# Optimization experiments

Measured on AMD Instinct MI355X. Metric: run time of the kernel, lower is better.

Reference implementation:

```python
import jax, jax.numpy as jnp
import numpy as np

B, F, H, S, K, L, C = 128, 8192, 8192, 4, 32, 3, 100  # batch, encoded feats, hidden, segments, synapses/seg, hidden layers, classes


def setup_inputs() -> dict:
    key = jax.random.key(0)
    k1, k2, k3, k4, k5, k6 = jax.random.split(key, 6)
    # binary encoded input activations (thermometer-coded tabular features)
    x = jax.random.randint(k1, (B, F), 0, 2).astype(jnp.float32)
    # sign weights in {-1,+1} for each synapse of each segment of each neuron
    signs0 = jnp.where(jax.random.bernoulli(k2, 0.5, (S, H, K)), 1.0, -1.0).astype(jnp.float32)
    signsH = jnp.where(jax.random.bernoulli(k3, 0.5, (L - 1, S, H, K)), 1.0, -1.0).astype(jnp.float32)
    # synapse source indices (irregular connectivity)
    idx0 = jax.random.randint(k4, (S, H, K), 0, F, dtype=jnp.int32)
    idxH = jax.random.randint(k5, (L - 1, S, H, K), 0, H, dtype=jnp.int32)
    # per-layer output connection matrices [L, H, C]
    wout = jax.random.normal(k6, (L, H, C), dtype=jnp.float32) * 0.02
    return {"x": x, "signs0": signs0, "signsH": signsH, "wout": wout,
            "idx0": idx0, "idxH": idxH, "threshold": 8}


def _segment_layer(a, idx, signs, threshold):
    # a: [B, P] prev activations; idx/signs: [S, H, K]
    g = a[:, idx]                                  # [B, S, H, K] irregular gather
    z = jnp.einsum('bshk,shk->bsh', g, signs)      # per-segment summed input
    fired = jnp.any(z >= threshold, axis=1)        # OR over segments -> [B, H]
    return fired.astype(a.dtype)


def reference(x, signs0, signsH, wout, idx0, idxH, threshold):
    thr = jnp.float32(threshold)
    a = _segment_layer(x, idx0, signs0, thr)       # hidden layer 0
    acts = [a]
    for l in range(idxH.shape[0]):                 # remaining hidden layers (fixed small L)
        a = _segment_layer(a, idxH[l], signsH[l], thr)
        acts.append(a)
    # sum class votes from every hidden layer's output connection matrix
    out = jnp.einsum('lbh,lhc->bc', jnp.stack(acts, 0), wout)  # [B, C]
    return out
```

## Files before the change

kernel.cpp:

```cpp
#include <hip/hip_runtime.h>
#include <stdint.h>

#define B 128
#define F 8192
#define H 8192
#define S 4
#define K 32
#define L 3
#define C 100

#define NBLK 256
#define NTHR 512


__device__ __forceinline__ int load_threshold(const int* p) {
    int v = *p;
    if (v >= (1 << 23)) v = (int)__int_as_float(v);
    return v;
}

__device__ __forceinline__ void cs5(uint32_t* a, uint32_t v) {
#pragma unroll
    for (int i = 0; i < 5; ++i) { const uint32_t t = a[i]; a[i] = t ^ v; v = t & v; }
}

__device__ __forceinline__ void pair_sum5(const uint32_t* x, uint32_t* y) {
    uint32_t c = 0;
#pragma unroll
    for (int i = 0; i < 5; ++i) {
        const uint32_t p = (uint32_t)__shfl_xor((int)x[i], 32);
        const uint32_t s = x[i] ^ p;
        y[i] = s ^ c;
        c = (x[i] & p) | (s & c);
    }
    y[5] = c;
}

__device__ __forceinline__ uint32_t fired_cmp(const uint32_t* A, const uint32_t* P, int thr) {
    uint32_t Y[7];
    uint32_t c = 0;
#pragma unroll
    for (int i = 0; i < 7; ++i) {
        const uint32_t ai = (i < 6) ? A[i] : 0u;
        const uint32_t bm = ((thr >> i) & 1) ? 0xFFFFFFFFu : 0u;
        const uint32_t t  = ai ^ bm;
        Y[i] = t ^ c;
        c = (ai & bm) | (t & c);
    }
    uint32_t bw = 0;
#pragma unroll
    for (int i = 0; i < 7; ++i) {
        const uint32_t xx = (i >= 1) ? P[i - 1] : 0u;
        const uint32_t d  = xx ^ Y[i];
        bw = ((~xx) & Y[i]) | ((~d) & bw);
    }
    return ~bw;
}

#define GLDS16(gp, lp)                                                \
    __builtin_amdgcn_global_load_lds(                                 \
        (const __attribute__((address_space(1))) uint32_t*)(gp),      \
        (__attribute__((address_space(3))) uint32_t*)(lp), 16, 0, 0)

#define AG_LOAD(p)                                                          \
    __hip_atomic_load((p), __ATOMIC_RELAXED, __HIP_MEMORY_SCOPE_AGENT)
#define AG_STORE(p, v)                                                      \
    __hip_atomic_store((p), (v), __ATOMIC_RELAXED, __HIP_MEMORY_SCOPE_AGENT)

__device__ __forceinline__ void wp_barrier(uint32_t* wbar, uint32_t ep,
                                           int tid, int gidx) {
    asm volatile("s_waitcnt vmcnt(0)" ::: "memory");
    __syncthreads();
    if (tid == 0) {
        const uint32_t t = __hip_atomic_fetch_add(&wbar[gidx * 16], 1u,
                               __ATOMIC_RELAXED, __HIP_MEMORY_SCOPE_AGENT) + 1u;
        if (t == ep * 16u) {
            const uint32_t r = __hip_atomic_fetch_add(&wbar[128], 1u,
                               __ATOMIC_RELAXED, __HIP_MEMORY_SCOPE_AGENT) + 1u;
            if (r == ep * 8u) AG_STORE(&wbar[160], ep);
        }
        int guard = 0;
        while (AG_LOAD(&wbar[160]) < ep) {
            __builtin_amdgcn_s_sleep(2);
            if (++guard > (1 << 17)) break;
        }
    }
    __syncthreads();
    asm volatile("" ::: "memory");
}

__device__ __forceinline__ void layer_phase(
        const uint32_t* __restrict__ prevPlane,
        const int* __restrict__ idx,
        const float* __restrict__ signs,
        uint32_t* __restrict__ outPlane,
        const int thr, const int hg, const int tid,
        uint2* tab, uint32_t* fbuf) {
    const int lane = tid & 63;
    const int ww   = tid >> 6;
    const int s    = ww & 3;
    const int rh   = ww >> 2;
    const int kh   = lane >> 5;
    const int h5   = lane & 31;
    const int hloc = rh * 32 + h5;
    const int h    = hg * 64 + hloc;

    const size_t gb = ((size_t)s * H + h) * K + kh * 16;
    const int4   i0 = *(const int4*)(idx + gb);
    const int4   i1 = *(const int4*)(idx + gb + 4);
    const int4   i2 = *(const int4*)(idx + gb + 8);
    const int4   i3 = *(const int4*)(idx + gb + 12);
    const float4 s0 = *(const float4*)(signs + gb);
    const float4 s1 = *(const float4*)(signs + gb + 4);
    const float4 s2 = *(const float4*)(signs + gb + 8);
    const float4 s3 = *(const float4*)(signs + gb + 12);

    {
        uint32_t* lbase = (uint32_t*)tab;
#pragma unroll
        for (int i = 0; i < 8; ++i) {
            const int o = (i * 512 + tid) * 4;
            GLDS16(prevPlane + o, lbase + o);
        }
    }
    __syncthreads();

    const uint32_t iv[16] = {
        (uint32_t)i0.x, (uint32_t)i0.y, (uint32_t)i0.z, (uint32_t)i0.w,
        (uint32_t)i1.x, (uint32_t)i1.y, (uint32_t)i1.z, (uint32_t)i1.w,
        (uint32_t)i2.x, (uint32_t)i2.y, (uint32_t)i2.z, (uint32_t)i2.w,
        (uint32_t)i3.x, (uint32_t)i3.y, (uint32_t)i3.z, (uint32_t)i3.w };
    const uint32_t pm[16] = {
        ~(uint32_t)(__float_as_int(s0.x) >> 31), ~(uint32_t)(__float_as_int(s0.y) >> 31),
        ~(uint32_t)(__float_as_int(s0.z) >> 31), ~(uint32_t)(__float_as_int(s0.w) >> 31),
        ~(uint32_t)(__float_as_int(s1.x) >> 31), ~(uint32_t)(__float_as_int(s1.y) >> 31),
        ~(uint32_t)(__float_as_int(s1.z) >> 31), ~(uint32_t)(__float_as_int(s1.w) >> 31),
        ~(uint32_t)(__float_as_int(s2.x) >> 31), ~(uint32_t)(__float_as_int(s2.y) >> 31),
        ~(uint32_t)(__float_as_int(s2.z) >> 31), ~(uint32_t)(__float_as_int(s2.w) >> 31),
        ~(uint32_t)(__float_as_int(s3.x) >> 31), ~(uint32_t)(__float_as_int(s3.y) >> 31),
        ~(uint32_t)(__float_as_int(s3.z) >> 31), ~(uint32_t)(__float_as_int(s3.w) >> 31) };

    uint32_t A0[5] = {0,0,0,0,0}, P0[5] = {0,0,0,0,0};
    uint32_t A1[5] = {0,0,0,0,0}, P1[5] = {0,0,0,0,0};
#pragma unroll
    for (int c8 = 0; c8 < 2; ++c8) {
        uint2 g[8];
#pragma unroll
        for (int j = 0; j < 8; ++j) g[j] = tab[iv[c8 * 8 + j]];
#pragma unroll
        for (int j = 0; j < 8; ++j) {
            const uint32_t pmv = pm[c8 * 8 + j];
            cs5(A0, g[j].x);
            cs5(P0, g[j].x & pmv);
            cs5(A1, g[j].y);
            cs5(P1, g[j].y & pmv);
        }
    }

    uint32_t A0f[6], P0f[6], A1f[6], P1f[6];
    pair_sum5(A0, A0f);
    pair_sum5(P0, P0f);
    pair_sum5(A1, A1f);
    pair_sum5(P1, P1f);

    const uint32_t f0 = fired_cmp(A0f, P0f, thr);
    const uint32_t f1 = fired_cmp(A1f, P1f, thr);

    if (kh == 0) {
        fbuf[((s * 2 + rh) * 32 + h5) * 2 + 0] = f0;
        fbuf[((s * 2 + rh) * 32 + h5) * 2 + 1] = f1;
    }
    __syncthreads();

    if (tid < 128) {
        const int rr   = tid >> 6;
        const int hh   = (tid >> 1) & 31;
        const int comp = tid & 1;
        uint32_t v = 0;
#pragma unroll
        for (int s2 = 0; s2 < 4; ++s2)
            v |= fbuf[((s2 * 2 + rr) * 32 + hh) * 2 + comp];
        AG_STORE(&outPlane[(size_t)(hg * 64 + rr * 32 + hh) * 2 + comp], v);
    }
}

__global__ __launch_bounds__(128) void init_pack_kernel(
        const float* __restrict__ x, uint2* __restrict__ xPP,
        float* __restrict__ out, uint32_t* __restrict__ bar) {
    const int zi = blockIdx.x * 128 + threadIdx.x;
    if (zi < B * C) out[zi] = 0.0f;
    if (blockIdx.x < 4) bar[blockIdx.x * 128 + threadIdx.x] = 0u;

    const int b  = threadIdx.x;
    const int wv = threadIdx.x >> 6;
    const int f0 = blockIdx.x * 32;
    const float4* xr = (const float4*)(x + (size_t)b * F + f0);
    for (int j = 0; j < 8; ++j) {
        const float4 v = xr[j];
        const uint64_t m0 = __ballot(v.x > 0.5f);
        const uint64_t m1 = __ballot(v.y > 0.5f);
        const uint64_t m2 = __ballot(v.z > 0.5f);
        const uint64_t m3 = __ballot(v.w > 0.5f);
        if ((threadIdx.x & 63) == 0) {
            const int f = f0 + 4 * j;
            uint4* dst = (uint4*)(xPP + (size_t)wv * F + f);
            dst[0] = make_uint4((uint32_t)m0, (uint32_t)(m0 >> 32),
                                (uint32_t)m1, (uint32_t)(m1 >> 32));
            dst[1] = make_uint4((uint32_t)m2, (uint32_t)(m2 >> 32),
                                (uint32_t)m3, (uint32_t)(m3 >> 32));
        }
    }
}

__global__ __launch_bounds__(512, 4) void fused_kernel(
        const uint32_t* __restrict__ xPP,
        const int* __restrict__ idx0, const float* __restrict__ signs0,
        const int* __restrict__ idxH, const float* __restrict__ signsH,
        const float* __restrict__ wout, const int* __restrict__ thrp,
        uint32_t* __restrict__ actPP, float* __restrict__ out,
        uint32_t* __restrict__ bar) {
    __shared__ uint2    tab[H];
    __shared__ uint32_t fbuf[4 * 2 * 32 * 2];

    const int tid = threadIdx.x;
    const int bid = blockIdx.x;
    const int wp  = bid & 1;
    const int hg  = bid >> 1;
    const int thr = load_threshold(thrp);

    uint32_t* wbar = bar + wp * 256;
    const int gidx = (bid >> 1) & 7;

    const uint32_t* xPlane = xPP + (size_t)wp * 2 * F;
    uint32_t* pl0 = actPP + (size_t)(0 * 2 + wp) * 2 * H;
    uint32_t* pl1 = actPP + (size_t)(1 * 2 + wp) * 2 * H;
    uint32_t* pl2 = actPP + (size_t)(2 * 2 + wp) * 2 * H;

    const int*   idx2   = idxH;
    const float* signs2 = signsH;
    const int*   idx3   = idxH + (size_t)S * H * K;
    const float* signs3 = signsH + (size_t)S * H * K;

    layer_phase(xPlane, idx0, signs0, pl0, thr, hg, tid, tab, fbuf);
    wp_barrier(wbar, 1, tid, gidx);

    layer_phase(pl0, idx2, signs2, pl1, thr, hg, tid, tab, fbuf);
    wp_barrier(wbar, 2, tid, gidx);

    layer_phase(pl1, idx3, signs3, pl2, thr, hg, tid, tab, fbuf);
    wp_barrier(wbar, 3, tid, gidx);

    {
        const int lane = tid & 63;
        const int gw   = bid * 8 + (tid >> 6);
        const int b    = gw >> 4;
        const int hc   = gw & 15;
        const int w32  = b >> 5;
        const int fwp  = w32 >> 1;
        const int comp = w32 & 1;
        const int bit  = b & 31;

        uint32_t mv[L][8];
#pragma unroll
        for (int l = 0; l < L; ++l) {
            const uint32_t* aT = actPP + (size_t)(l * 2 + fwp) * 2 * H + comp;
#pragma unroll
            for (int r = 0; r < 8; ++r)
                mv[l][r] = AG_LOAD(&aT[(size_t)(hc * 512 + r * 64 + lane) * 2]);
        }

        float acc0 = 0.0f, acc1 = 0.0f;
        const int c1 = 64 + lane;
        const bool c1v = (c1 < C);

#pragma unroll
        for (int l = 0; l < L; ++l) {
            const float* wl = wout + (size_t)l * H * C;
#pragma unroll
            for (int r = 0; r < 8; ++r) {
                const int hbase = hc * 512 + r * 64;
                uint64_t hm = __ballot((mv[l][r] >> bit) & 1u);
                while (hm) {
                    const int slot = __ffsll((unsigned long long)hm) - 1;
                    hm &= hm - 1;
                    const float* wr = wl + (size_t)(hbase + slot) * C;
                    acc0 += wr[lane];
                    if (c1v) acc1 += wr[c1];
                }
            }
        }
        atomicAdd(&out[b * C + lane], acc0);
        if (c1v) atomicAdd(&out[b * C + c1], acc1);
    }
}

extern "C" void kernel_launch(void* const* d_in, const int* in_sizes, int n_in,
                              void* d_out, int out_size, void* d_ws, size_t ws_size,
                              hipStream_t stream) {
    const float* x      = (const float*)d_in[0];
    const float* signs0 = (const float*)d_in[1];
    const float* signsH = (const float*)d_in[2];
    const float* wout   = (const float*)d_in[3];
    const int*   idx0   = (const int*)d_in[4];
    const int*   idxH   = (const int*)d_in[5];
    const int*   thr    = (const int*)d_in[6];
    float* out = (float*)d_out;

    uint32_t* xPP   = (uint32_t*)d_ws;
    uint32_t* actPP = xPP + (size_t)4 * F;
    uint32_t* bar   = actPP + (size_t)12 * H;
    uint2*    xPP2  = (uint2*)d_ws;

    init_pack_kernel<<<F / 32, 128, 0, stream>>>(x, xPP2, out, bar);
    fused_kernel<<<NBLK, NTHR, 0, stream>>>(xPP, idx0, signs0, idxH, signsH,
                                            wout, thr, actPP, out, bar);
}
```

Measured before the change: 129.2 us.

## Fold input packing into fused kernel and overlap activation loads with layers

Removes the separate init/pack kernel launch by having the persistent fused kernel zero the output, pack input bits, and reset barrier counters itself, adding an extra grid barrier gated by a magic-word handshake. The per-layer activation bitmasks for the output stage are loaded right after each layer's barrier rather than all at the end, overlapping them with later layers. Barrier release flags are spread over per-group cache lines, and the output accumulation loop batches up to eight weight-row loads for more memory-level parallelism. This adds an extra grid-wide sync, plus risk from the in-kernel counter reset racing with barrier arrivals and a stale magic word persisting across calls.

```diff
diff --git a/kernel.cpp b/kernel.cpp
--- a/kernel.cpp
+++ b/kernel.cpp
@@ -67,22 +67,38 @@
 #define AG_STORE(p, v)                                                      \
     __hip_atomic_store((p), (v), __ATOMIC_RELAXED, __HIP_MEMORY_SCOPE_AGENT)
 
-__device__ __forceinline__ void wp_barrier(uint32_t* wbar, uint32_t ep,
-                                           int tid, int gidx) {
+#define MAGIC_A 0x3C6EF372u
+#define MAGIC_B 0xDAA66D2Bu
+#define MAG_IDX 2048
+
+__device__ __forceinline__ void wp_barrier(uint32_t* bar, int wp, uint32_t ep,
+                                           int tid, int gidx, bool first) {
     asm volatile("s_waitcnt vmcnt(0)" ::: "memory");
     __syncthreads();
     if (tid == 0) {
-        const uint32_t t = __hip_atomic_fetch_add(&wbar[gidx * 16], 1u,
+        uint32_t* wbar = bar + wp * 1024;
+        int guard = 0;
+        if (first) {
+            while (AG_LOAD(&bar[MAG_IDX]) != MAGIC_A ||
+                   AG_LOAD(&bar[MAG_IDX + 1]) != MAGIC_B) {
+                __builtin_amdgcn_s_sleep(2);
+                if (++guard > (1 << 18)) break;
+            }
+        }
+        const uint32_t t = __hip_atomic_fetch_add(&wbar[gidx * 32], 1u,
                                __ATOMIC_RELAXED, __HIP_MEMORY_SCOPE_AGENT) + 1u;
         if (t == ep * 16u) {
-            const uint32_t r = __hip_atomic_fetch_add(&wbar[128], 1u,
+            const uint32_t r = __hip_atomic_fetch_add(&wbar[256], 1u,
                                __ATOMIC_RELAXED, __HIP_MEMORY_SCOPE_AGENT) + 1u;
-            if (r == ep * 8u) AG_STORE(&wbar[160], ep);
-        }
-        int guard = 0;
-        while (AG_LOAD(&wbar[160]) < ep) {
+            if (r == ep * 8u) {
+#pragma unroll
+                for (int g = 0; g < 8; ++g) AG_STORE(&wbar[512 + g * 32], ep);
+            }
+        }
+        guard = 0;
+        while (AG_LOAD(&wbar[512 + gidx * 32]) < ep) {
             __builtin_amdgcn_s_sleep(2);
-            if (++guard > (1 << 17)) break;
+            if (++guard > (1 << 18)) break;
         }
     }
     __syncthreads();
@@ -102,8 +118,7 @@
     const int rh   = ww >> 2;
     const int kh   = lane >> 5;
     const int h5   = lane & 31;
-    const int hloc = rh * 32 + h5;
-    const int h    = hg * 64 + hloc;
+    const int h    = hg * 64 + rh * 32 + h5;
 
     const size_t gb = ((size_t)s * H + h) * K + kh * 16;
     const int4   i0 = *(const int4*)(idx + gb);
@@ -184,39 +199,12 @@
     }
 }
 
-__global__ __launch_bounds__(128) void init_pack_kernel(
-        const float* __restrict__ x, uint2* __restrict__ xPP,
-        float* __restrict__ out, uint32_t* __restrict__ bar) {
-    const int zi = blockIdx.x * 128 + threadIdx.x;
-    if (zi < B * C) out[zi] = 0.0f;
-    if (blockIdx.x < 4) bar[blockIdx.x * 128 + threadIdx.x] = 0u;
-
-    const int b  = threadIdx.x;
-    const int wv = threadIdx.x >> 6;
-    const int f0 = blockIdx.x * 32;
-    const float4* xr = (const float4*)(x + (size_t)b * F + f0);
-    for (int j = 0; j < 8; ++j) {
-        const float4 v = xr[j];
-        const uint64_t m0 = __ballot(v.x > 0.5f);
-        const uint64_t m1 = __ballot(v.y > 0.5f);
-        const uint64_t m2 = __ballot(v.z > 0.5f);
-        const uint64_t m3 = __ballot(v.w > 0.5f);
-        if ((threadIdx.x & 63) == 0) {
-            const int f = f0 + 4 * j;
-            uint4* dst = (uint4*)(xPP + (size_t)wv * F + f);
-            dst[0] = make_uint4((uint32_t)m0, (uint32_t)(m0 >> 32),
-                                (uint32_t)m1, (uint32_t)(m1 >> 32));
-            dst[1] = make_uint4((uint32_t)m2, (uint32_t)(m2 >> 32),
-                                (uint32_t)m3, (uint32_t)(m3 >> 32));
-        }
-    }
-}
-
 __global__ __launch_bounds__(512, 4) void fused_kernel(
-        const uint32_t* __restrict__ xPP,
+        const float* __restrict__ x,
         const int* __restrict__ idx0, const float* __restrict__ signs0,
         const int* __restrict__ idxH, const float* __restrict__ signsH,
         const float* __restrict__ wout, const int* __restrict__ thrp,
+        uint32_t* __restrict__ xPP,
         uint32_t* __restrict__ actPP, float* __restrict__ out,
         uint32_t* __restrict__ bar) {
     __shared__ uint2    tab[H];
@@ -226,49 +214,98 @@
     const int bid = blockIdx.x;
     const int wp  = bid & 1;
     const int hg  = bid >> 1;
+    const int gidx = hg & 7;
     const int thr = load_threshold(thrp);
 
-    uint32_t* wbar = bar + wp * 256;
-    const int gidx = (bid >> 1) & 7;
+    if (bid == 0) {
+#pragma unroll
+        for (int i = 0; i < 4; ++i) AG_STORE(&bar[i * 512 + tid], 0u);
+        asm volatile("s_waitcnt vmcnt(0)" ::: "memory");
+        __syncthreads();
+        if (tid == 0) {
+            AG_STORE(&bar[MAG_IDX], MAGIC_A);
+            AG_STORE(&bar[MAG_IDX + 1], MAGIC_B);
+        }
+    }
+
+    {
+        const int zi = bid * 512 + tid;
+        if (zi < B * C) AG_STORE((uint32_t*)&out[zi], 0u);
+
+        const int b   = tid & 127;
+        const int wv  = (tid >> 6) & 1;
+        const int sub = tid >> 7;
+        const int f0  = bid * 32;
+        const float4* xr = (const float4*)(x + (size_t)b * F + f0);
+#pragma unroll
+        for (int jj = 0; jj < 2; ++jj) {
+            const int j = sub * 2 + jj;
+            const float4 v = xr[j];
+            const uint64_t m0 = __ballot(v.x > 0.5f);
+            const uint64_t m1 = __ballot(v.y > 0.5f);
+            const uint64_t m2 = __ballot(v.z > 0.5f);
+            const uint64_t m3 = __ballot(v.w > 0.5f);
+            if ((tid & 63) == 0) {
+                const int f = f0 + 4 * j;
+                unsigned long long* q =
+                    (unsigned long long*)(xPP + ((size_t)wv * F + f) * 2);
+                AG_STORE(q + 0, (unsigned long long)m0);
+                AG_STORE(q + 1, (unsigned long long)m1);
+                AG_STORE(q + 2, (unsigned long long)m2);
+                AG_STORE(q + 3, (unsigned long long)m3);
+            }
+        }
+    }
+    wp_barrier(bar, wp, 1, tid, gidx, true);
 
     const uint32_t* xPlane = xPP + (size_t)wp * 2 * F;
     uint32_t* pl0 = actPP + (size_t)(0 * 2 + wp) * 2 * H;
     uint32_t* pl1 = actPP + (size_t)(1 * 2 + wp) * 2 * H;
     uint32_t* pl2 = actPP + (size_t)(2 * 2 + wp) * 2 * H;
-
     const int*   idx2   = idxH;
     const float* signs2 = signsH;
     const int*   idx3   = idxH + (size_t)S * H * K;
     const float* signs3 = signsH + (size_t)S * H * K;
 
+    const int lane = tid & 63;
+    const int gw   = bid * 8 + (tid >> 6);
+    const int fb   = gw >> 4;
+    const int hc   = gw & 15;
+    const int w32  = fb >> 5;
+    const int fwp  = w32 >> 1;
+    const int comp = w32 & 1;
+    const int bit  = fb & 31;
+    uint32_t mv[L][8];
+
     layer_phase(xPlane, idx0, signs0, pl0, thr, hg, tid, tab, fbuf);
-    wp_barrier(wbar, 1, tid, gidx);
-
+    wp_barrier(bar, wp, 2, tid, gidx, false);
+
+    {
+        const uint32_t* aT = actPP + (size_t)(0 * 2 + fwp) * 2 * H + comp;
+#pragma unroll
+        for (int r = 0; r < 8; ++r)
+            mv[0][r] = AG_LOAD(&aT[(size_t)(hc * 512 + r * 64 + lane) * 2]);
+    }
     layer_phase(pl0, idx2, signs2, pl1, thr, hg, tid, tab, fbuf);
-    wp_barrier(wbar, 2, tid, gidx);
-
+    wp_barrier(bar, wp, 3, tid, gidx, false);
+
+    {
+        const uint32_t* aT = actPP + (size_t)(1 * 2 + fwp) * 2 * H + comp;
+#pragma unroll
+        for (int r = 0; r < 8; ++r)
+            mv[1][r] = AG_LOAD(&aT[(size_t)(hc * 512 + r * 64 + lane) * 2]);
+    }
     layer_phase(pl1, idx3, signs3, pl2, thr, hg, tid, tab, fbuf);
-    wp_barrier(wbar, 3, tid, gidx);
-
-    {
-        const int lane = tid & 63;
-        const int gw   = bid * 8 + (tid >> 6);
-        const int b    = gw >> 4;
-        const int hc   = gw & 15;
-        const int w32  = b >> 5;
-        const int fwp  = w32 >> 1;
-        const int comp = w32 & 1;
-        const int bit  = b & 31;
-
-        uint32_t mv[L][8];
-#pragma unroll
-        for (int l = 0; l < L; ++l) {
-            const uint32_t* aT = actPP + (size_t)(l * 2 + fwp) * 2 * H + comp;
-#pragma unroll
-            for (int r = 0; r < 8; ++r)
-                mv[l][r] = AG_LOAD(&aT[(size_t)(hc * 512 + r * 64 + lane) * 2]);
-        }
-
+    wp_barrier(bar, wp, 4, tid, gidx, false);
+
+    {
+        const uint32_t* aT = actPP + (size_t)(2 * 2 + fwp) * 2 * H + comp;
+#pragma unroll
+        for (int r = 0; r < 8; ++r)
+            mv[2][r] = AG_LOAD(&aT[(size_t)(hc * 512 + r * 64 + lane) * 2]);
+    }
+
+    {
         float acc0 = 0.0f, acc1 = 0.0f;
         const int c1 = 64 + lane;
         const bool c1v = (c1 < C);
@@ -281,16 +318,28 @@
                 const int hbase = hc * 512 + r * 64;
                 uint64_t hm = __ballot((mv[l][r] >> bit) & 1u);
                 while (hm) {
-                    const int slot = __ffsll((unsigned long long)hm) - 1;
-                    hm &= hm - 1;
-                    const float* wr = wl + (size_t)(hbase + slot) * C;
-                    acc0 += wr[lane];
-                    if (c1v) acc1 += wr[c1];
+                    int sl[8];
+#pragma unroll
+                    for (int i = 0; i < 8; ++i) {
+                        sl[i] = hm ? (__ffsll((unsigned long long)hm) - 1) : -1;
+                        hm &= hm - 1;
+                    }
+                    float v0[8], v1[8];
+#pragma unroll
+                    for (int i = 0; i < 8; ++i) {
+                        if (sl[i] >= 0) {
+                            const float* wr = wl + (size_t)(hbase + sl[i]) * C;
+                            v0[i] = wr[lane];
+                            v1[i] = c1v ? wr[c1] : 0.0f;
+                        } else { v0[i] = 0.0f; v1[i] = 0.0f; }
+                    }
+#pragma unroll
+                    for (int i = 0; i < 8; ++i) { acc0 += v0[i]; acc1 += v1[i]; }
                 }
             }
         }
-        atomicAdd(&out[b * C + lane], acc0);
-        if (c1v) atomicAdd(&out[b * C + c1], acc1);
+        atomicAdd(&out[fb * C + lane], acc0);
+        if (c1v) atomicAdd(&out[fb * C + c1], acc1);
     }
 }
 
@@ -309,9 +358,7 @@
     uint32_t* xPP   = (uint32_t*)d_ws;
     uint32_t* actPP = xPP + (size_t)4 * F;
     uint32_t* bar   = actPP + (size_t)12 * H;
-    uint2*    xPP2  = (uint2*)d_ws;
-
-    init_pack_kernel<<<F / 32, 128, 0, stream>>>(x, xPP2, out, bar);
-    fused_kernel<<<NBLK, NTHR, 0, stream>>>(xPP, idx0, signs0, idxH, signsH,
-                                            wout, thr, actPP, out, bar);
-}
+
+    fused_kernel<<<NBLK, NTHR, 0, stream>>>(x, idx0, signs0, idxH, signsH,
+                                            wout, thr, xPP, actPP, out, bar);
+}
```

Result: faster. 118.6 us (-8.2%).

## Use single grid-wide barrier with per-group flags, prefetch activations, unroll weight gather

Applied to the files above, without the earlier changes.

Replaces the two independent per-batch-half barriers with one grid-wide barrier over all 256 blocks. Blocks count into 8 group counters, and the release flag is replicated into 8 separate cache lines so pollers spread across them. Layer-0 and layer-1 activation words for the output stage are loaded before the last barrier, and the popcount-driven wout gather is unrolled four slots at a time to expose more memory-level parallelism. The change risks extra barrier latency, because every block now waits for the whole grid rather than only its batch half.

```diff
diff --git a/kernel.cpp b/kernel.cpp
--- a/kernel.cpp
+++ b/kernel.cpp
@@ -67,22 +67,25 @@
 #define AG_STORE(p, v)                                                      \
     __hip_atomic_store((p), (v), __ATOMIC_RELAXED, __HIP_MEMORY_SCOPE_AGENT)
 
-__device__ __forceinline__ void wp_barrier(uint32_t* wbar, uint32_t ep,
-                                           int tid, int gidx) {
+__device__ __forceinline__ void grid_barrier(uint32_t* bar, uint32_t ep,
+                                             int tid, int gidx) {
     asm volatile("s_waitcnt vmcnt(0)" ::: "memory");
     __syncthreads();
     if (tid == 0) {
-        const uint32_t t = __hip_atomic_fetch_add(&wbar[gidx * 16], 1u,
+        const uint32_t t = __hip_atomic_fetch_add(&bar[gidx * 32], 1u,
                                __ATOMIC_RELAXED, __HIP_MEMORY_SCOPE_AGENT) + 1u;
-        if (t == ep * 16u) {
-            const uint32_t r = __hip_atomic_fetch_add(&wbar[128], 1u,
+        if (t == ep * 32u) {
+            const uint32_t r = __hip_atomic_fetch_add(&bar[256], 1u,
                                __ATOMIC_RELAXED, __HIP_MEMORY_SCOPE_AGENT) + 1u;
-            if (r == ep * 8u) AG_STORE(&wbar[160], ep);
+            if (r == ep * 8u) {
+#pragma unroll
+                for (int g = 0; g < 8; ++g) AG_STORE(&bar[512 + g * 32], ep);
+            }
         }
         int guard = 0;
-        while (AG_LOAD(&wbar[160]) < ep) {
+        while (AG_LOAD(&bar[512 + gidx * 32]) < ep) {
             __builtin_amdgcn_s_sleep(2);
-            if (++guard > (1 << 17)) break;
+            if (++guard > (1 << 18)) break;
         }
     }
     __syncthreads();
@@ -102,8 +105,7 @@
     const int rh   = ww >> 2;
     const int kh   = lane >> 5;
     const int h5   = lane & 31;
-    const int hloc = rh * 32 + h5;
-    const int h    = hg * 64 + hloc;
+    const int h    = hg * 64 + rh * 32 + h5;
 
     const size_t gb = ((size_t)s * H + h) * K + kh * 16;
     const int4   i0 = *(const int4*)(idx + gb);
@@ -189,7 +191,7 @@
         float* __restrict__ out, uint32_t* __restrict__ bar) {
     const int zi = blockIdx.x * 128 + threadIdx.x;
     if (zi < B * C) out[zi] = 0.0f;
-    if (blockIdx.x < 4) bar[blockIdx.x * 128 + threadIdx.x] = 0u;
+    if (blockIdx.x < 8) bar[blockIdx.x * 128 + threadIdx.x] = 0u;
 
     const int b  = threadIdx.x;
     const int wv = threadIdx.x >> 6;
@@ -226,49 +228,53 @@
     const int bid = blockIdx.x;
     const int wp  = bid & 1;
     const int hg  = bid >> 1;
+    const int gidx = bid & 7;
     const int thr = load_threshold(thrp);
-
-    uint32_t* wbar = bar + wp * 256;
-    const int gidx = (bid >> 1) & 7;
 
     const uint32_t* xPlane = xPP + (size_t)wp * 2 * F;
     uint32_t* pl0 = actPP + (size_t)(0 * 2 + wp) * 2 * H;
     uint32_t* pl1 = actPP + (size_t)(1 * 2 + wp) * 2 * H;
     uint32_t* pl2 = actPP + (size_t)(2 * 2 + wp) * 2 * H;
-
     const int*   idx2   = idxH;
     const float* signs2 = signsH;
     const int*   idx3   = idxH + (size_t)S * H * K;
     const float* signs3 = signsH + (size_t)S * H * K;
 
     layer_phase(xPlane, idx0, signs0, pl0, thr, hg, tid, tab, fbuf);
-    wp_barrier(wbar, 1, tid, gidx);
+    grid_barrier(bar, 1, tid, gidx);
 
     layer_phase(pl0, idx2, signs2, pl1, thr, hg, tid, tab, fbuf);
-    wp_barrier(wbar, 2, tid, gidx);
+    grid_barrier(bar, 2, tid, gidx);
 
     layer_phase(pl1, idx3, signs3, pl2, thr, hg, tid, tab, fbuf);
-    wp_barrier(wbar, 3, tid, gidx);
+
+    const int lane = tid & 63;
+    const int gw   = bid * 8 + (tid >> 6);
+    const int fb   = gw >> 4;
+    const int hc   = gw & 15;
+    const int w32  = fb >> 5;
+    const int fwp  = w32 >> 1;
+    const int comp = w32 & 1;
+    const int bit  = fb & 31;
+
+    uint32_t mv[L][8];
+#pragma unroll
+    for (int l = 0; l < 2; ++l) {
+        const uint32_t* aT = actPP + (size_t)(l * 2 + fwp) * 2 * H + comp;
+#pragma unroll
+        for (int r = 0; r < 8; ++r)
+            mv[l][r] = AG_LOAD(&aT[(size_t)(hc * 512 + r * 64 + lane) * 2]);
+    }
+    grid_barrier(bar, 3, tid, gidx);
 
     {
-        const int lane = tid & 63;
-        const int gw   = bid * 8 + (tid >> 6);
-        const int b    = gw >> 4;
-        const int hc   = gw & 15;
-        const int w32  = b >> 5;
-        const int fwp  = w32 >> 1;
-        const int comp = w32 & 1;
-        const int bit  = b & 31;
-
-        uint32_t mv[L][8];
-#pragma unroll
-        for (int l = 0; l < L; ++l) {
-            const uint32_t* aT = actPP + (size_t)(l * 2 + fwp) * 2 * H + comp;
-#pragma unroll
-            for (int r = 0; r < 8; ++r)
-                mv[l][r] = AG_LOAD(&aT[(size_t)(hc * 512 + r * 64 + lane) * 2]);
-        }
-
+        const uint32_t* aT = actPP + (size_t)(2 * 2 + fwp) * 2 * H + comp;
+#pragma unroll
+        for (int r = 0; r < 8; ++r)
+            mv[2][r] = AG_LOAD(&aT[(size_t)(hc * 512 + r * 64 + lane) * 2]);
+    }
+
+    {
         float acc0 = 0.0f, acc1 = 0.0f;
         const int c1 = 64 + lane;
         const bool c1v = (c1 < C);
@@ -281,16 +287,39 @@
                 const int hbase = hc * 512 + r * 64;
                 uint64_t hm = __ballot((mv[l][r] >> bit) & 1u);
                 while (hm) {
-                    const int slot = __ffsll((unsigned long long)hm) - 1;
-                    hm &= hm - 1;
-                    const float* wr = wl + (size_t)(hbase + slot) * C;
-                    acc0 += wr[lane];
-                    if (c1v) acc1 += wr[c1];
+                    const int sa = __ffsll((unsigned long long)hm) - 1; hm &= hm - 1;
+                    const int sb = __ffsll((unsigned long long)hm) - 1; hm &= hm - 1;
+                    const int sc = __ffsll((unsigned long long)hm) - 1; hm &= hm - 1;
+                    const int sd = __ffsll((unsigned long long)hm) - 1; hm &= hm - 1;
+                    float a0, a1 = 0.0f, b0 = 0.0f, b1 = 0.0f;
+                    float c0 = 0.0f, c1f = 0.0f, d0 = 0.0f, d1 = 0.0f;
+                    {
+                        const float* w = wl + (size_t)(hbase + sa) * C;
+                        a0 = w[lane];
+                        if (c1v) a1 = w[c1];
+                    }
+                    if (sb >= 0) {
+                        const float* w = wl + (size_t)(hbase + sb) * C;
+                        b0 = w[lane];
+                        if (c1v) b1 = w[c1];
+                    }
+                    if (sc >= 0) {
+                        const float* w = wl + (size_t)(hbase + sc) * C;
+                        c0 = w[lane];
+                        if (c1v) c1f = w[c1];
+                    }
+                    if (sd >= 0) {
+                        const float* w = wl + (size_t)(hbase + sd) * C;
+                        d0 = w[lane];
+                        if (c1v) d1 = w[c1];
+                    }
+                    acc0 += (a0 + b0) + (c0 + d0);
+                    acc1 += (a1 + b1) + (c1f + d1);
                 }
             }
         }
-        atomicAdd(&out[b * C + lane], acc0);
-        if (c1v) atomicAdd(&out[b * C + c1], acc1);
+        atomicAdd(&out[fb * C + lane], acc0);
+        if (c1v) atomicAdd(&out[fb * C + c1], acc1);
     }
 }
 
```

New measurement: 119.8 us. -7.3%, faster.
